# Performance work log

Measured on AMD Instinct MI355X. Metric: run time of the kernel, lower is better.

The kernel has to match this reference:

```python
import jax, jax.numpy as jnp
import numpy as np

TEMPERATURE = 0.1
EPS = 1e-12  # matches torch F.normalize eps


def setup_inputs() -> dict:
    key = jax.random.key(0)
    k1, k2 = jax.random.split(key)
    B, T, C = 8, 1024, 512
    x = jax.random.normal(k1, (B, T, C), dtype=jnp.float32)
    quantized = jax.random.normal(k2, (B, T, C), dtype=jnp.float32)
    return {"x": x, "quantized": quantized}


def reference(x, quantized):
    B, T, C = x.shape
    xf = x.reshape(-1, C)            # (N, C)
    qf = quantized.reshape(-1, C)    # (N, C)
    xn = xf / jnp.maximum(jnp.linalg.norm(xf, axis=-1, keepdims=True), EPS)
    qn = qf / jnp.maximum(jnp.linalg.norm(qf, axis=-1, keepdims=True), EPS)
    # (N, N) similarity logits
    sim = jnp.matmul(xn, qn.T) / TEMPERATURE
    N = sim.shape[0]
    # cross-entropy with targets = arange(N): loss_i = logsumexp(sim_i) - sim_ii
    logZ = jax.nn.logsumexp(sim, axis=-1)
    diag = jnp.diagonal(sim)
    loss = jnp.mean(logZ - diag)
    predictions = jnp.argmax(sim, axis=-1)
    targets = jnp.arange(N)
    accuracy = jnp.mean((predictions == targets).astype(jnp.float32))
    return loss, accuracy
```

## Files before the change

kernel.cpp:

```cpp
#include <hip/hip_runtime.h>
#include <hip/hip_bf16.h>
#include <math.h>

#define CDIM 512
#define NROW 8192
#define BM 256
#define BN 128
#define BK 32
#define NT 16
#define NCB 64
#define BUFSZ 24576
#define TEMP_INV 10.0f

typedef unsigned short u16;
typedef u16  u16x8 __attribute__((ext_vector_type(8)));
typedef __bf16 bf16x8 __attribute__((ext_vector_type(8)));
typedef float  f32x4 __attribute__((ext_vector_type(4)));

static __device__ __forceinline__ float bf2f(u16 u) {
    return __uint_as_float(((unsigned)u) << 16);
}
static __device__ __forceinline__ u16 f2bf(float f) {
    unsigned u = __float_as_uint(f);
    return (u16)((u + 0x7FFFu + ((u >> 16) & 1u)) >> 16);
}

static __device__ __forceinline__ void gload_lds16(const u16* g, char* l) {
    __builtin_amdgcn_global_load_lds(
        (const __attribute__((address_space(1))) void*)g,
        (__attribute__((address_space(3))) void*)l, 16, 0, 0);
}

__global__ __launch_bounds__(256) void norm_split_kernel(
    const float* __restrict__ x, const float* __restrict__ q,
    u16* __restrict__ xh, u16* __restrict__ qh, int n)
{
    int wave = blockIdx.x * 4 + (threadIdx.x >> 6);
    int lane = threadIdx.x & 63;
    const float* src; u16* dh; int row;
    if (wave < n) { src = x; dh = xh; row = wave; }
    else          { src = q; dh = qh; row = wave - n; }

    const float4* p = reinterpret_cast<const float4*>(src + (size_t)row * CDIM);
    float4 a = p[lane * 2];
    float4 b = p[lane * 2 + 1];
    float v[8] = {a.x, a.y, a.z, a.w, b.x, b.y, b.z, b.w};
    float ss = 0.f;
#pragma unroll
    for (int j = 0; j < 8; ++j) ss += v[j] * v[j];
#pragma unroll
    for (int off = 32; off; off >>= 1) ss += __shfl_xor(ss, off);
    float scale = 1.0f / fmaxf(sqrtf(ss), 1e-12f);

    u16 h[8] __attribute__((aligned(16)));
#pragma unroll
    for (int j = 0; j < 8; ++j) h[j] = f2bf(v[j] * scale);
    *(u16x8*)&dh[(size_t)row * CDIM + lane * 8] = *(u16x8*)h;
}

__global__ __launch_bounds__(512, 4) void sim_main_kernel(
    const u16* __restrict__ xh, const u16* __restrict__ qh,
    float4* __restrict__ part)
{
    extern __shared__ __align__(16) char smem[];
    const int t = threadIdx.x, lane = t & 63, wid = t >> 6;
    const int wm = wid >> 1, wn = wid & 1;

    const int orig = blockIdx.x;
    const int wg = (orig & 7) * 256 + (orig >> 3);
    const int rb = wg & 31, cb = wg >> 5;
    const int row0 = rb * BM, col0 = cb * BN;

    const int schunk = (t & 3) ^ ((t >> 3) & 3);
    const u16* sa0 = xh + (size_t)(row0 + (t >> 2)) * CDIM + schunk * 8;
    const u16* sa1 = sa0 + 128 * CDIM;
    const u16* sb  = qh + (size_t)(col0 + (t >> 2)) * CDIM + schunk * 8;
    const unsigned dstw = (unsigned)wid * 1024u;

    auto stage = [&](int kt) {
        char* b = smem + (kt % 3) * BUFSZ;
        const int ko = kt * BK;
        gload_lds16(sa0 + ko, b + dstw);
        gload_lds16(sa1 + ko, b + 8192 + dstw);
        gload_lds16(sb  + ko, b + 16384 + dstw);
    };

    const unsigned kxc = ((unsigned)((lane >> 4) ^ ((lane >> 1) & 3))) * 16u;
    const unsigned aro = ((unsigned)(wm * 64 + (lane & 15))) * 64u + kxc;
    const unsigned bro = 16384u + ((unsigned)(wn * 64 + (lane & 15))) * 64u + kxc;

    f32x4 acc[4][4];
#pragma unroll
    for (int i = 0; i < 4; ++i)
#pragma unroll
        for (int j = 0; j < 4; ++j) acc[i][j] = (f32x4){0.f, 0.f, 0.f, 0.f};

    stage(0); stage(1);
    asm volatile("s_waitcnt vmcnt(3)" ::: "memory");
    __builtin_amdgcn_s_barrier();
    asm volatile("" ::: "memory");

    for (int kt = 0; kt < NT; ++kt) {
        const char* buf = smem + (kt % 3) * BUFSZ;
        if (kt < NT - 2) stage(kt + 2);
        bf16x8 afr[4], bfr[4];
#pragma unroll
        for (int mf = 0; mf < 4; ++mf) afr[mf] = *(const bf16x8*)(buf + aro + mf * 1024u);
#pragma unroll
        for (int nf = 0; nf < 4; ++nf) bfr[nf] = *(const bf16x8*)(buf + bro + nf * 1024u);

        __builtin_amdgcn_s_setprio(1);
#pragma unroll
        for (int mf = 0; mf < 4; ++mf)
#pragma unroll
            for (int nf = 0; nf < 4; ++nf)
                acc[mf][nf] = __builtin_amdgcn_mfma_f32_16x16x32_bf16(
                    afr[mf], bfr[nf], acc[mf][nf], 0, 0, 0);
        __builtin_amdgcn_s_setprio(0);

        if (kt < NT - 2)       { asm volatile("s_waitcnt vmcnt(3)" ::: "memory"); }
        else if (kt == NT - 2) { asm volatile("s_waitcnt vmcnt(0)" ::: "memory"); }
        asm volatile("s_waitcnt lgkmcnt(0)" ::: "memory");
        __builtin_amdgcn_s_barrier();
        asm volatile("" ::: "memory");
    }

    __syncthreads();
    float* sm = (float*)smem;
    float* sl = sm + 512;
    int*   si = (int*)(sl + 512);
    float* sd = (float*)(si + 512);
    const int g = lane >> 4;
#pragma unroll
    for (int mf = 0; mf < 4; ++mf) {
#pragma unroll
        for (int r = 0; r < 4; ++r) {
            const int row_loc  = wm * 64 + mf * 16 + g * 4 + r;
            const int row_glob = row0 + row_loc;
            const int ci = col0 + wn * 64 + (lane & 15);
            float vmax = acc[mf][0][r];
            int cbest = ci;
#pragma unroll
            for (int nf = 1; nf < 4; ++nf) {
                float v = acc[mf][nf][r];
                if (v > vmax) { vmax = v; cbest = ci + nf * 16; }
                if (ci + nf * 16 == row_glob) sd[row_loc] = v * TEMP_INV;
            }
            if (ci == row_glob) sd[row_loc] = acc[mf][0][r] * TEMP_INV;
#pragma unroll
            for (int m = 1; m < 16; m <<= 1) {
                float ov = __shfl_xor(vmax, m);
                int   oi = __shfl_xor(cbest, m);
                if (ov > vmax || (ov == vmax && oi < cbest)) { vmax = ov; cbest = oi; }
            }
            float s = 0.f;
#pragma unroll
            for (int nf = 0; nf < 4; ++nf)
                s += __expf((acc[mf][nf][r] - vmax) * TEMP_INV);
#pragma unroll
            for (int m = 1; m < 16; m <<= 1) s += __shfl_xor(s, m);
            if ((lane & 15) == 0) {
                sm[row_loc * 2 + wn] = vmax * TEMP_INV;
                sl[row_loc * 2 + wn] = s;
                si[row_loc * 2 + wn] = cbest;
            }
        }
    }
    __syncthreads();
    if (t < 256) {
        float m0 = sm[t * 2], m1 = sm[t * 2 + 1];
        float M = fmaxf(m0, m1);
        float L = sl[t * 2] * __expf(m0 - M) + sl[t * 2 + 1] * __expf(m1 - M);
        int bi = (m1 > m0) ? si[t * 2 + 1] : si[t * 2];
        part[(size_t)(row0 + t) * NCB + cb] =
            make_float4(M, L, __int_as_float(bi), sd[t]);
    }
}

__global__ __launch_bounds__(256) void merge_kernel(
    const float4* __restrict__ part,
    float* __restrict__ loss_arr, float* __restrict__ corr_arr)
{
    int i    = blockIdx.x * 4 + (threadIdx.x >> 6);
    int lane = threadIdx.x & 63;
    float4 v = part[(size_t)i * NCB + lane];

    float M = v.x;
#pragma unroll
    for (int off = 32; off; off >>= 1) M = fmaxf(M, __shfl_xor(M, off));
    float L = v.y * __expf(v.x - M);
#pragma unroll
    for (int off = 32; off; off >>= 1) L += __shfl_xor(L, off);
    float bm = v.x; int bi = __float_as_int(v.z);
#pragma unroll
    for (int off = 1; off < 64; off <<= 1) {
        float ov = __shfl_xor(bm, off);
        int   oi = __shfl_xor(bi, off);
        if (ov > bm || (ov == bm && oi < bi)) { bm = ov; bi = oi; }
    }
    float dg = __shfl(v.w, i >> 7);
    if (lane == 0) {
        loss_arr[i] = (M + logf(L)) - dg;
        corr_arr[i] = (bi == i) ? 1.0f : 0.0f;
    }
}

__global__ __launch_bounds__(256) void finalize_kernel(
    const float* __restrict__ loss_arr, const float* __restrict__ corr_arr,
    float* __restrict__ out, int n)
{
    float a = 0.f, b = 0.f;
    for (int i = threadIdx.x; i < n; i += 256) { a += loss_arr[i]; b += corr_arr[i]; }
#pragma unroll
    for (int off = 32; off; off >>= 1) { a += __shfl_xor(a, off); b += __shfl_xor(b, off); }
    __shared__ float sa[4], sb[4];
    int wid = threadIdx.x >> 6, lane = threadIdx.x & 63;
    if (lane == 0) { sa[wid] = a; sb[wid] = b; }
    __syncthreads();
    if (threadIdx.x == 0) {
        out[0] = (sa[0] + sa[1] + sa[2] + sa[3]) / n;
        out[1] = (sb[0] + sb[1] + sb[2] + sb[3]) / n;
    }
}

extern "C" void kernel_launch(void* const* d_in, const int* in_sizes, int n_in,
                              void* d_out, int out_size, void* d_ws, size_t ws_size,
                              hipStream_t stream)
{
    const float* x = (const float*)d_in[0];
    const float* q = (const float*)d_in[1];
    const int n = in_sizes[0] / CDIM;

    char* ws = (char*)d_ws;
    size_t sz_bf = (size_t)n * CDIM * sizeof(u16);
    u16* xh = (u16*)(ws);
    u16* qh = (u16*)(ws + sz_bf);
    char* p = ws + 2 * sz_bf;
    float4* part = (float4*)p; p += (size_t)n * NCB * sizeof(float4);
    float* loss_arr = (float*)p; p += (size_t)n * 4;
    float* corr_arr = (float*)p;

    norm_split_kernel<<<(2 * n) / 4, 256, 0, stream>>>(x, q, xh, qh, n);

    sim_main_kernel<<<(n / BM) * (n / BN), 512, 3 * BUFSZ, stream>>>(xh, qh, part);

    merge_kernel<<<n / 4, 256, 0, stream>>>(part, loss_arr, corr_arr);

    finalize_kernel<<<1, 256, 0, stream>>>(loss_arr, corr_arr, (float*)d_out, n);
}
```

Baseline: 134.5 us.

## Enlarge GEMM tile to 256x256 with 16 waves and XCD-aware block mapping

Doubles the column tile of the fused similarity/softmax kernel from 128 to 256, using 1024-thread blocks (16 waves arranged 4x4) so each block loads one A and one B chunk per thread per k-step. This raises arithmetic intensity and halves the number of column partials, so the merge kernel reads 32 partials per row instead of 64. Block-to-tile mapping is changed so each XCD handles a contiguous group of column blocks, aiming at better L2 reuse of B. The cost is larger LDS per block (96KB), which likely limits blocks per CU, and a bigger per-block epilogue.

```diff
diff --git a/kernel.cpp b/kernel.cpp
--- a/kernel.cpp
+++ b/kernel.cpp
@@ -5,11 +5,11 @@
 #define CDIM 512
 #define NROW 8192
 #define BM 256
-#define BN 128
+#define BN 256
 #define BK 32
 #define NT 16
-#define NCB 64
-#define BUFSZ 24576
+#define NCB 32
+#define BUFSZ 32768
 #define TEMP_INV 10.0f
 
 typedef unsigned short u16;
@@ -58,31 +58,30 @@
     *(u16x8*)&dh[(size_t)row * CDIM + lane * 8] = *(u16x8*)h;
 }
 
-__global__ __launch_bounds__(512, 4) void sim_main_kernel(
+__global__ __launch_bounds__(1024, 4) void sim_main_kernel(
     const u16* __restrict__ xh, const u16* __restrict__ qh,
     float4* __restrict__ part)
 {
     extern __shared__ __align__(16) char smem[];
     const int t = threadIdx.x, lane = t & 63, wid = t >> 6;
-    const int wm = wid >> 1, wn = wid & 1;
+    const int wm = wid >> 2, wn = wid & 3;
 
     const int orig = blockIdx.x;
-    const int wg = (orig & 7) * 256 + (orig >> 3);
-    const int rb = wg & 31, cb = wg >> 5;
+    const int xcd = orig & 7, s = orig >> 3;
+    const int rb = s >> 2;
+    const int cb = xcd * 4 + (s & 3);
     const int row0 = rb * BM, col0 = cb * BN;
 
     const int schunk = (t & 3) ^ ((t >> 3) & 3);
-    const u16* sa0 = xh + (size_t)(row0 + (t >> 2)) * CDIM + schunk * 8;
-    const u16* sa1 = sa0 + 128 * CDIM;
-    const u16* sb  = qh + (size_t)(col0 + (t >> 2)) * CDIM + schunk * 8;
+    const u16* sa = xh + (size_t)(row0 + (t >> 2)) * CDIM + schunk * 8;
+    const u16* sb = qh + (size_t)(col0 + (t >> 2)) * CDIM + schunk * 8;
     const unsigned dstw = (unsigned)wid * 1024u;
 
     auto stage = [&](int kt) {
         char* b = smem + (kt % 3) * BUFSZ;
         const int ko = kt * BK;
-        gload_lds16(sa0 + ko, b + dstw);
-        gload_lds16(sa1 + ko, b + 8192 + dstw);
-        gload_lds16(sb  + ko, b + 16384 + dstw);
+        gload_lds16(sa + ko, b + dstw);
+        gload_lds16(sb + ko, b + 16384 + dstw);
     };
 
     const unsigned kxc = ((unsigned)((lane >> 4) ^ ((lane >> 1) & 3))) * 16u;
@@ -96,7 +95,7 @@
         for (int j = 0; j < 4; ++j) acc[i][j] = (f32x4){0.f, 0.f, 0.f, 0.f};
 
     stage(0); stage(1);
-    asm volatile("s_waitcnt vmcnt(3)" ::: "memory");
+    asm volatile("s_waitcnt vmcnt(2)" ::: "memory");
     __builtin_amdgcn_s_barrier();
     asm volatile("" ::: "memory");
 
@@ -118,7 +117,7 @@
                     afr[mf], bfr[nf], acc[mf][nf], 0, 0, 0);
         __builtin_amdgcn_s_setprio(0);
 
-        if (kt < NT - 2)       { asm volatile("s_waitcnt vmcnt(3)" ::: "memory"); }
+        if (kt < NT - 2)       { asm volatile("s_waitcnt vmcnt(2)" ::: "memory"); }
         else if (kt == NT - 2) { asm volatile("s_waitcnt vmcnt(0)" ::: "memory"); }
         asm volatile("s_waitcnt lgkmcnt(0)" ::: "memory");
         __builtin_amdgcn_s_barrier();
@@ -127,9 +126,9 @@
 
     __syncthreads();
     float* sm = (float*)smem;
-    float* sl = sm + 512;
-    int*   si = (int*)(sl + 512);
-    float* sd = (float*)(si + 512);
+    float* sl = sm + 1024;
+    int*   si = (int*)(sl + 1024);
+    float* sd = (float*)(si + 1024);
     const int g = lane >> 4;
 #pragma unroll
     for (int mf = 0; mf < 4; ++mf) {
@@ -153,25 +152,33 @@
                 int   oi = __shfl_xor(cbest, m);
                 if (ov > vmax || (ov == vmax && oi < cbest)) { vmax = ov; cbest = oi; }
             }
-            float s = 0.f;
+            float ssum = 0.f;
 #pragma unroll
             for (int nf = 0; nf < 4; ++nf)
-                s += __expf((acc[mf][nf][r] - vmax) * TEMP_INV);
-#pragma unroll
-            for (int m = 1; m < 16; m <<= 1) s += __shfl_xor(s, m);
+                ssum += __expf((acc[mf][nf][r] - vmax) * TEMP_INV);
+#pragma unroll
+            for (int m = 1; m < 16; m <<= 1) ssum += __shfl_xor(ssum, m);
             if ((lane & 15) == 0) {
-                sm[row_loc * 2 + wn] = vmax * TEMP_INV;
-                sl[row_loc * 2 + wn] = s;
-                si[row_loc * 2 + wn] = cbest;
+                sm[row_loc * 4 + wn] = vmax * TEMP_INV;
+                sl[row_loc * 4 + wn] = ssum;
+                si[row_loc * 4 + wn] = cbest;
             }
         }
     }
     __syncthreads();
     if (t < 256) {
-        float m0 = sm[t * 2], m1 = sm[t * 2 + 1];
-        float M = fmaxf(m0, m1);
-        float L = sl[t * 2] * __expf(m0 - M) + sl[t * 2 + 1] * __expf(m1 - M);
-        int bi = (m1 > m0) ? si[t * 2 + 1] : si[t * 2];
+        float M = sm[t * 4];
+#pragma unroll
+        for (int w = 1; w < 4; ++w) M = fmaxf(M, sm[t * 4 + w]);
+        float L = 0.f;
+#pragma unroll
+        for (int w = 0; w < 4; ++w) L += sl[t * 4 + w] * __expf(sm[t * 4 + w] - M);
+        float bv = -1e30f; int bi = 0;
+#pragma unroll
+        for (int w = 0; w < 4; ++w) {
+            float v = sm[t * 4 + w];
+            if (v > bv) { bv = v; bi = si[t * 4 + w]; }
+        }
         part[(size_t)(row0 + t) * NCB + cb] =
             make_float4(M, L, __int_as_float(bi), sd[t]);
     }
@@ -183,22 +190,22 @@
 {
     int i    = blockIdx.x * 4 + (threadIdx.x >> 6);
     int lane = threadIdx.x & 63;
-    float4 v = part[(size_t)i * NCB + lane];
+    float4 v = part[(size_t)i * NCB + (lane & 31)];
 
     float M = v.x;
 #pragma unroll
     for (int off = 32; off; off >>= 1) M = fmaxf(M, __shfl_xor(M, off));
-    float L = v.y * __expf(v.x - M);
+    float L = (lane < 32) ? v.y * __expf(v.x - M) : 0.f;
 #pragma unroll
     for (int off = 32; off; off >>= 1) L += __shfl_xor(L, off);
     float bm = v.x; int bi = __float_as_int(v.z);
 #pragma unroll
-    for (int off = 1; off < 64; off <<= 1) {
+    for (int off = 1; off < 32; off <<= 1) {
         float ov = __shfl_xor(bm, off);
         int   oi = __shfl_xor(bi, off);
         if (ov > bm || (ov == bm && oi < bi)) { bm = ov; bi = oi; }
     }
-    float dg = __shfl(v.w, i >> 7);
+    float dg = __shfl(v.w, i >> 8);
     if (lane == 0) {
         loss_arr[i] = (M + logf(L)) - dg;
         corr_arr[i] = (bi == i) ? 1.0f : 0.0f;
@@ -242,7 +249,7 @@
 
     norm_split_kernel<<<(2 * n) / 4, 256, 0, stream>>>(x, q, xh, qh, n);
 
-    sim_main_kernel<<<(n / BM) * (n / BN), 512, 3 * BUFSZ, stream>>>(xh, qh, part);
+    sim_main_kernel<<<(n / BM) * (n / BN), 1024, 3 * BUFSZ, stream>>>(xh, qh, part);
 
     merge_kernel<<<n / 4, 256, 0, stream>>>(part, loss_arr, corr_arr);
 
```

Result: faster. 122.6 us (median of 6 runs) (-8.9%).
